# Optimization experiments

Hardware: AMD Instinct MI355X
Metric: run time of the kernel (lower is better)

Reference implementation:

```python
import jax, jax.numpy as jnp
import numpy as np

D_MODEL = 2048
N_HEADS = 16
N_KV_HEADS = 4
D_K = D_MODEL // N_HEADS          # 128
N_REP = N_HEADS // N_KV_HEADS     # 4
MAX_SEQ_LEN = 2048


def _rope_tables():
    # Matches torch Rotary: d_k//4 geometric freqs followed by d_k//4 zeros.
    freqs = (1.0 / 10000.0) ** jnp.linspace(0.0, 1.0, D_K // 4, dtype=jnp.float32)
    freqs = jnp.concatenate([freqs, jnp.zeros(D_K // 4, dtype=jnp.float32)])
    t = jnp.arange(MAX_SEQ_LEN, dtype=jnp.float32)
    theta = t[:, None] * freqs[None, :]          # [max_seq_len, d_k//2]
    return jnp.cos(theta), jnp.sin(theta)


def _apply_rotary(x, cos, sin):
    # Faithful to original: x is (B, H, T, D) and the table is indexed by
    # x.size(-3) == H (the original code rotates per-HEAD, broadcast over time).
    H = x.shape[1]
    c = cos[None, :H, None, :]
    s = sin[None, :H, None, :]
    xf = x.astype(jnp.float32)
    x1, x2 = jnp.split(xf, 2, axis=-1)
    y1 = x1 * c + x2 * s
    y2 = -x1 * s + x2 * c
    return jnp.concatenate([y1, y2], axis=-1).astype(x.dtype)


def setup_inputs() -> dict:
    key = jax.random.key(0)
    ks = jax.random.split(key, 5)
    B, T = 2, 2048
    scale = 1.0 / np.sqrt(D_MODEL)
    x = jax.random.normal(ks[0], (B, T, D_MODEL), dtype=jnp.float32)
    wq = jax.random.normal(ks[1], (N_HEADS * D_K, D_MODEL), dtype=jnp.float32) * scale
    wk = jax.random.normal(ks[2], (N_KV_HEADS * D_K, D_MODEL), dtype=jnp.float32) * scale
    wv = jax.random.normal(ks[3], (N_KV_HEADS * D_K, D_MODEL), dtype=jnp.float32) * scale
    wo = jax.random.normal(ks[4], (D_MODEL, D_MODEL), dtype=jnp.float32) * scale
    return {"x": x, "wq": wq, "wk": wk, "wv": wv, "wo": wo}


def reference(x, wq, wk, wv, wo):
    B, T, _ = x.shape
    cos, sin = _rope_tables()

    Q = (x @ wq.T).reshape(B, T, N_HEADS, D_K).transpose(0, 2, 1, 3)      # (B,Hq,T,D)
    K = (x @ wk.T).reshape(B, T, N_KV_HEADS, D_K).transpose(0, 2, 1, 3)   # (B,Hkv,T,D)
    V = (x @ wv.T).reshape(B, T, N_KV_HEADS, D_K).transpose(0, 2, 1, 3)

    Q = _apply_rotary(Q, cos, sin)
    K = _apply_rotary(K, cos, sin)

    # repeat_interleave over head dim to match query heads
    K = jnp.repeat(K, N_REP, axis=1)   # (B,Hq,T,D)
    V = jnp.repeat(V, N_REP, axis=1)

    scale = 1.0 / jnp.sqrt(jnp.asarray(D_K, dtype=jnp.float32))
    scores = jnp.einsum('bhqd,bhkd->bhqk', Q, K) * scale
    causal = jnp.tril(jnp.ones((T, T), dtype=bool))
    scores = jnp.where(causal[None, None, :, :], scores, jnp.finfo(scores.dtype).min)
    attn = jax.nn.softmax(scores, axis=-1)
    out = jnp.einsum('bhqk,bhkd->bhqd', attn, V)          # (B,Hq,T,D)
    out = out.transpose(0, 2, 1, 3).reshape(B, T, D_MODEL)
    return out @ wo.T
```

## Files before the change

### kernel.cpp

```cpp
#include <hip/hip_runtime.h>
#include <cstdint>
#include <cstddef>

typedef __attribute__((ext_vector_type(8))) short bf16x8;
typedef __attribute__((ext_vector_type(4))) float f32x4;
typedef __attribute__((ext_vector_type(16))) float f32x16;
typedef unsigned short ushort_t;

#define MFMA_BF16(a, b, c) __builtin_amdgcn_mfma_f32_16x16x32_bf16((a), (b), (c), 0, 0, 0)
#define MFMA32_BF16(a, b, c) __builtin_amdgcn_mfma_f32_32x32x16_bf16((a), (b), (c), 0, 0, 0)

__device__ __forceinline__ unsigned short f2bf(float f) {
  unsigned int u = __float_as_uint(f);
  u += 0x7fffu + ((u >> 16) & 1u);
  return (unsigned short)(u >> 16);
}
__device__ __forceinline__ float bf2f(unsigned short h) {
  return __uint_as_float(((unsigned int)h) << 16);
}
__device__ __forceinline__ float exp2_fast(float x) {
  float r;
  asm("v_exp_f32 %0, %1" : "=v"(r) : "v"(x));
  return r;
}
__device__ __forceinline__ uint32_t cvtpk_bf16(float lo, float hi) {
  uint32_t r;
  asm("v_cvt_pk_bf16_f32 %0, %1, %2" : "=v"(r) : "v"(lo), "v"(hi));
  return r;
}

__device__ __forceinline__ void gload_lds16(const void* g, void* lds) {
  __builtin_amdgcn_global_load_lds(
      (const __attribute__((address_space(1))) void*)g,
      (__attribute__((address_space(3))) void*)lds, 16, 0, 0);
}

__global__ __launch_bounds__(256)
void cvt_kernel(const float* __restrict__ x, const float* __restrict__ wq,
                const float* __restrict__ wk, const float* __restrict__ wv,
                const float* __restrict__ wo,
                ushort_t* __restrict__ xb, ushort_t* __restrict__ wqb,
                ushort_t* __restrict__ wkb, ushort_t* __restrict__ wvb,
                ushort_t* __restrict__ wob) {
  const float* src; ushort_t* dst; int n;
  switch (blockIdx.y) {
    case 0:  src = x;  dst = xb;  n = 8388608; break;
    case 1:  src = wq; dst = wqb; n = 4194304; break;
    case 2:  src = wk; dst = wkb; n = 1048576; break;
    case 3:  src = wv; dst = wvb; n = 1048576; break;
    default: src = wo; dst = wob; n = 4194304; break;
  }
  const int i = (int)(blockIdx.x * 256u + threadIdx.x) * 4;
  if (i >= n) return;
  const float4 v = *(const float4*)(src + i);
  union { unsigned short us[4]; unsigned long long u64; } pk;
  pk.us[0] = f2bf(v.x); pk.us[1] = f2bf(v.y);
  pk.us[2] = f2bf(v.z); pk.us[3] = f2bf(v.w);
  *(unsigned long long*)(dst + i) = pk.u64;
}

__global__ __launch_bounds__(256, 2)
void gemm_qkv(const ushort_t* __restrict__ A,
              const ushort_t* __restrict__ WQ, const ushort_t* __restrict__ WK,
              const ushort_t* __restrict__ WV,
              ushort_t* __restrict__ Qb, ushort_t* __restrict__ Kb,
              ushort_t* __restrict__ Vtb) {
  __shared__ bf16x8 smem_v[4096];
  char* smem = (char*)smem_v;
  const int tid  = threadIdx.x;
  const int lane = tid & 63;
  const int wave = tid >> 6;
  const int wr = wave >> 1, wc = wave & 1;
  const int y = blockIdx.y;
  int mode, ylocal;
  const ushort_t* Bsel;
  if (y < 16)      { mode = 0; ylocal = y;      Bsel = WQ; }
  else if (y < 20) { mode = 1; ylocal = y - 16; Bsel = WK; }
  else             { mode = 2; ylocal = y - 20; Bsel = WV; }
  const ushort_t* Abase = A + (size_t)blockIdx.x * 128 * 2048;
  const ushort_t* Bbase = Bsel + (size_t)ylocal * 128 * 2048;

  f32x4 acc[4][4] = {};

  #pragma unroll
  for (int it = 0; it < 4; ++it) {
    const int chunk = it * 4 + wave;
    const int r  = chunk * 8 + (lane >> 3);
    const int cg = (lane & 7) ^ (r & 7);
    gload_lds16(Abase + (size_t)r * 2048 + cg * 8, smem + chunk * 1024);
    gload_lds16(Bbase + (size_t)r * 2048 + cg * 8, smem + 16384 + chunk * 1024);
  }
  __syncthreads();

  for (int t = 0; t < 32; ++t) {
    if (t + 1 < 32) {
      char* dst = smem + ((t + 1) & 1) * 32768;
      const int k0 = (t + 1) * 64;
      #pragma unroll
      for (int it = 0; it < 4; ++it) {
        const int chunk = it * 4 + wave;
        const int r  = chunk * 8 + (lane >> 3);
        const int cg = (lane & 7) ^ (r & 7);
        gload_lds16(Abase + (size_t)r * 2048 + k0 + cg * 8, dst + chunk * 1024);
        gload_lds16(Bbase + (size_t)r * 2048 + k0 + cg * 8, dst + 16384 + chunk * 1024);
      }
    }

    char* As = smem + (t & 1) * 32768;
    char* Bs = As + 16384;
    bf16x8 af[2][4], bf_[2][4];
    #pragma unroll
    for (int kki = 0; kki < 2; ++kki) {
      #pragma unroll
      for (int m = 0; m < 4; ++m) {
        const int row = wr * 64 + m * 16 + (lane & 15);
        const int cg  = ((kki << 2) + (lane >> 4)) ^ (row & 7);
        af[kki][m] = *(const bf16x8*)(As + row * 128 + cg * 16);
      }
      #pragma unroll
      for (int n = 0; n < 4; ++n) {
        const int row = wc * 64 + n * 16 + (lane & 15);
        const int cg  = ((kki << 2) + (lane >> 4)) ^ (row & 7);
        bf_[kki][n] = *(const bf16x8*)(Bs + row * 128 + cg * 16);
      }
    }
    #pragma unroll
    for (int kki = 0; kki < 2; ++kki)
      #pragma unroll
      for (int m = 0; m < 4; ++m)
        #pragma unroll
        for (int n = 0; n < 4; ++n)
          acc[m][n] = MFMA_BF16(af[kki][m], bf_[kki][n], acc[m][n]);

    __syncthreads();
  }

  const int row0 = blockIdx.x * 128 + wr * 64;
  const int col0 = ylocal * 128 + wc * 64;
  #pragma unroll
  for (int m = 0; m < 4; ++m) {
    #pragma unroll
    for (int n = 0; n < 4; ++n) {
      #pragma unroll
      for (int j = 0; j < 4; ++j) {
        const int gm = row0 + m * 16 + ((lane >> 4) << 2) + j;
        const int gn = col0 + n * 16 + (lane & 15);
        const float v = acc[m][n][j];
        if (mode == 0) {
          Qb[(size_t)gm * 2048 + gn] = f2bf(v);
        } else if (mode == 1) {
          Kb[(size_t)gm * 512 + gn] = f2bf(v);
        } else {
          const int bb = gm >> 11, t2 = gm & 2047;
          Vtb[(size_t)bb * 512 * 2048 + (size_t)gn * 2048 + t2] = f2bf(v);
        }
      }
    }
  }
}

template<int WMODE>
__global__ __launch_bounds__(256, 2)
void gemm_bt(const ushort_t* __restrict__ A, const ushort_t* __restrict__ B,
             void* __restrict__ Cout, int M, int N, int K) {
  __shared__ bf16x8 smem_v[4096];
  char* smem = (char*)smem_v;
  const int tid  = threadIdx.x;
  const int lane = tid & 63;
  const int wave = tid >> 6;
  const int wr = wave >> 1, wc = wave & 1;
  const ushort_t* Abase = A + (size_t)blockIdx.x * 128 * K;
  const ushort_t* Bbase = B + (size_t)blockIdx.y * 128 * K;

  f32x4 acc[4][4] = {};
  const int nk = K >> 6;

  #pragma unroll
  for (int it = 0; it < 4; ++it) {
    const int chunk = it * 4 + wave;
    const int r  = chunk * 8 + (lane >> 3);
    const int cg = (lane & 7) ^ (r & 7);
    gload_lds16(Abase + (size_t)r * K + cg * 8, smem + chunk * 1024);
    gload_lds16(Bbase + (size_t)r * K + cg * 8, smem + 16384 + chunk * 1024);
  }
  __syncthreads();

  for (int t = 0; t < nk; ++t) {
    if (t + 1 < nk) {
      char* dst = smem + ((t + 1) & 1) * 32768;
      const int k0 = (t + 1) * 64;
      #pragma unroll
      for (int it = 0; it < 4; ++it) {
        const int chunk = it * 4 + wave;
        const int r  = chunk * 8 + (lane >> 3);
        const int cg = (lane & 7) ^ (r & 7);
        gload_lds16(Abase + (size_t)r * K + k0 + cg * 8, dst + chunk * 1024);
        gload_lds16(Bbase + (size_t)r * K + k0 + cg * 8, dst + 16384 + chunk * 1024);
      }
    }

    char* As = smem + (t & 1) * 32768;
    char* Bs = As + 16384;
    bf16x8 af[2][4], bf_[2][4];
    #pragma unroll
    for (int kki = 0; kki < 2; ++kki) {
      #pragma unroll
      for (int m = 0; m < 4; ++m) {
        const int row = wr * 64 + m * 16 + (lane & 15);
        const int cg  = ((kki << 2) + (lane >> 4)) ^ (row & 7);
        af[kki][m] = *(const bf16x8*)(As + row * 128 + cg * 16);
      }
      #pragma unroll
      for (int n = 0; n < 4; ++n) {
        const int row = wc * 64 + n * 16 + (lane & 15);
        const int cg  = ((kki << 2) + (lane >> 4)) ^ (row & 7);
        bf_[kki][n] = *(const bf16x8*)(Bs + row * 128 + cg * 16);
      }
    }
    #pragma unroll
    for (int kki = 0; kki < 2; ++kki)
      #pragma unroll
      for (int m = 0; m < 4; ++m)
        #pragma unroll
        for (int n = 0; n < 4; ++n)
          acc[m][n] = MFMA_BF16(af[kki][m], bf_[kki][n], acc[m][n]);

    __syncthreads();
  }

  const int row0 = blockIdx.x * 128 + wr * 64;
  const int col0 = blockIdx.y * 128 + wc * 64;
  #pragma unroll
  for (int m = 0; m < 4; ++m) {
    #pragma unroll
    for (int n = 0; n < 4; ++n) {
      #pragma unroll
      for (int j = 0; j < 4; ++j) {
        const int gm = row0 + m * 16 + ((lane >> 4) << 2) + j;
        const int gn = col0 + n * 16 + (lane & 15);
        const float v = acc[m][n][j];
        if (WMODE == 0) {
          ((ushort_t*)Cout)[(size_t)gm * N + gn] = f2bf(v);
        } else if (WMODE == 1) {
          ((float*)Cout)[(size_t)gm * N + gn] = v;
        } else {
          const int bb = gm >> 11, t2 = gm & 2047;
          ((ushort_t*)Cout)[(size_t)bb * N * 2048 + (size_t)gn * 2048 + t2] = f2bf(v);
        }
      }
    }
  }
}

__global__ __launch_bounds__(256)
void rope_k_kernel(ushort_t* __restrict__ K) {
  const int idx = blockIdx.x * 256 + threadIdx.x;
  const int NK = 4096 * 4 * 32;
  if (idx >= NK) return;
  const int t = idx >> 7, r = idx & 127;
  const int h = r >> 5, i = r & 31;
  ushort_t* p = K + (size_t)t * 512 + h * 128;
  const float f  = powf(10000.0f, -(float)i / 31.0f);
  const float th = (float)h * f;
  float sn, cs;
  sincosf(th, &sn, &cs);
  const float x1 = bf2f(p[i]), x2 = bf2f(p[i + 64]);
  p[i]      = f2bf(x1 * cs + x2 * sn);
  p[i + 64] = f2bf(-x1 * sn + x2 * cs);
}

__global__ __launch_bounds__(256, 2)
void attn_kernel(const ushort_t* __restrict__ Q, const ushort_t* __restrict__ K,
                 const ushort_t* __restrict__ Vt, ushort_t* __restrict__ AO) {
  __shared__ bf16x8 smem_v[4096];
  char* smem = (char*)smem_v;
  const int tid  = threadIdx.x;
  const int lane = tid & 63;
  const int wq   = tid >> 6;
  const int ql   = lane & 31;
  const int hi   = lane >> 5;

  const int lin = (int)blockIdx.x + 16 * (int)blockIdx.y + 256 * (int)blockIdx.z;
  const int xcd = lin & 7;
  const int s   = lin >> 3;
  const int b   = xcd >> 2;
  const int kh  = xcd & 3;
  const int h   = (kh << 2) + (s & 3);
  const int s4  = s >> 2;
  const int qt  = (s4 < 8) ? s4 : (23 - s4);

  const int q0b = qt * 128;
  const int qmin_w = q0b + wq * 32;
  const int qmax_w = qmin_w + 31;
  const int qrow = qmin_w + ql;

  const ushort_t* Qp = Q  + (size_t)b * 2048 * 2048 + (size_t)h  * 128;
  const ushort_t* Kp = K  + (size_t)b * 2048 * 512  + (size_t)kh * 128;
  const ushort_t* Vp = Vt + (size_t)b * 512 * 2048  + (size_t)kh * 128 * 2048;

  const int ntiles = (qt + 1) * 2;

  int offK[4], offV[4], ldK[4], ldV[4];
  #pragma unroll
  for (int it = 0; it < 4; ++it) {
    const int ck = it * 4 + wq;
    const int rK = ck * 4 + (lane >> 4);
    const int gK = (lane & 15) ^ (rK & 7);
    offK[it] = rK * 512 + gK * 8;  ldK[it] = ck * 1024;
    const int rV = ck * 8 + (lane >> 3);
    const int gV = (lane & 7) ^ (rV & 7);
    offV[it] = rV * 2048 + gV * 8; ldV[it] = 16384 + ck * 1024;
  }

  #pragma unroll
  for (int it = 0; it < 4; ++it) {
    gload_lds16(Kp + offK[it], smem + ldK[it]);
    gload_lds16(Vp + offV[it], smem + ldV[it]);
  }

  const float SCL = 0.08838834764831845f * 1.4426950408889634f;
  bf16x8 qf[8];
  #pragma unroll
  for (int ks = 0; ks < 8; ++ks)
    qf[ks] = *(const bf16x8*)(Qp + (size_t)qrow * 2048 + ks * 16 + hi * 8);
  #pragma unroll
  for (int ks = 0; ks < 2; ++ks) {
    union { bf16x8 v; ushort_t us[8]; } X1, X2;
    X1.v = qf[ks]; X2.v = qf[ks + 4];
    #pragma unroll
    for (int e = 0; e < 8; ++e) {
      const int i = ks * 16 + hi * 8 + e;
      const float f = __expf(-(float)i * (9.2103403720f / 31.0f));
      float sn, cs;
      sincosf((float)h * f, &sn, &cs);
      const float x1 = bf2f(X1.us[e]), x2 = bf2f(X2.us[e]);
      X1.us[e] = f2bf((x1 * cs + x2 * sn) * SCL);
      X2.us[e] = f2bf((-x1 * sn + x2 * cs) * SCL);
    }
    qf[ks] = X1.v; qf[ks + 4] = X2.v;
  }
  #pragma unroll
  for (int ks = 2; ks < 4; ++ks) {
    union { bf16x8 v; ushort_t us[8]; } X1, X2;
    X1.v = qf[ks]; X2.v = qf[ks + 4];
    #pragma unroll
    for (int e = 0; e < 8; ++e) {
      X1.us[e] = f2bf(bf2f(X1.us[e]) * SCL);
      X2.us[e] = f2bf(bf2f(X2.us[e]) * SCL);
    }
    qf[ks] = X1.v; qf[ks + 4] = X2.v;
  }

  float m_ = -3.0e38f, l_ = 0.f;
  f32x16 oacc[4] = {};

  __syncthreads();

  for (int ti = 0; ti < ntiles; ++ti) {
    const int kv0 = ti * 64;
    if (ti + 1 < ntiles) {
      const ushort_t* Kt = Kp + (size_t)(kv0 + 64) * 512;
      const ushort_t* Vn = Vp + (kv0 + 64);
      char* dst = smem + ((ti + 1) & 1) * 32768;
      #pragma unroll
      for (int it = 0; it < 4; ++it) {
        gload_lds16(Kt + offK[it], dst + ldK[it]);
        gload_lds16(Vn + offV[it], dst + ldV[it]);
      }
    }

    char* Ks = smem + (ti & 1) * 32768;
    char* Vs = Ks + 16384;
    if (kv0 <= qmax_w) {
      f32x16 sacc[2] = {};
      __builtin_amdgcn_s_setprio(1);
      #pragma unroll
      for (int kg = 0; kg < 2; ++kg) {
        const int key = kg * 32 + ql;
        #pragma unroll
        for (int ks = 0; ks < 8; ++ks) {
          const int g = ((ks << 1) + hi) ^ (key & 7);
          const bf16x8 kf = *(const bf16x8*)(Ks + key * 256 + g * 16);
          sacc[kg] = MFMA32_BF16(kf, qf[ks], sacc[kg]);
        }
      }
      __builtin_amdgcn_s_setprio(0);

      bf16x8 vfr[4][4];
      #pragma unroll
      for (int dg = 0; dg < 4; ++dg) {
        const int d = dg * 32 + ql;
        #pragma unroll
        for (int ks = 0; ks < 4; ++ks) {
          const int g = ((ks << 1) + hi) ^ (d & 7);
          vfr[dg][ks] = *(const bf16x8*)(Vs + d * 128 + g * 16);
        }
      }

      if (kv0 + 63 > qmin_w) {
        #pragma unroll
        for (int kg = 0; kg < 2; ++kg)
          #pragma unroll
          for (int r = 0; r < 16; ++r) {
            const int keyg = kv0 + kg * 32 + (r & 3) + 8 * (r >> 2) + 4 * hi;
            if (keyg > qrow) sacc[kg][r] = -3.0e38f;
          }
      }

      float mx[8];
      #pragma unroll
      for (int i = 0; i < 8; ++i) {
        const int kg = i >> 2, base = (i & 3) * 4;
        mx[i] = fmaxf(fmaxf(sacc[kg][base], sacc[kg][base + 1]),
                      fmaxf(sacc[kg][base + 2], sacc[kg][base + 3]));
      }
      float pm = fmaxf(fmaxf(fmaxf(mx[0], mx[1]), fmaxf(mx[2], mx[3])),
                       fmaxf(fmaxf(mx[4], mx[5]), fmaxf(mx[6], mx[7])));
      pm = fmaxf(pm, __shfl_xor(pm, 32));

      if (__any(pm > m_ + 11.0f)) {
        const float mn = fmaxf(m_, pm);
        const float alpha = exp2_fast(m_ - mn);
        m_ = mn;
        l_ *= alpha;
        #pragma unroll
        for (int r = 0; r < 16; ++r) {
          const float ar = __shfl(alpha, (r & 3) + 8 * (r >> 2) + 4 * hi);
          #pragma unroll
          for (int dg = 0; dg < 4; ++dg) oacc[dg][r] *= ar;
        }
      }

      float rs0 = 0.f, rs1 = 0.f, rs2 = 0.f, rs3 = 0.f;
      #pragma unroll
      for (int kg = 0; kg < 2; ++kg)
        #pragma unroll
        for (int r = 0; r < 16; r += 4) {
          const float p0 = exp2_fast(sacc[kg][r]     - m_);
          const float p1 = exp2_fast(sacc[kg][r + 1] - m_);
          const float p2 = exp2_fast(sacc[kg][r + 2] - m_);
          const float p3 = exp2_fast(sacc[kg][r + 3] - m_);
          sacc[kg][r] = p0; sacc[kg][r + 1] = p1;
          sacc[kg][r + 2] = p2; sacc[kg][r + 3] = p3;
          rs0 += p0; rs1 += p1; rs2 += p2; rs3 += p3;
        }
      float rs = (rs0 + rs1) + (rs2 + rs3);
      rs += __shfl_xor(rs, 32);
      l_ += rs;

      bf16x8 pa[4];
      #pragma unroll
      for (int ks = 0; ks < 4; ++ks) {
        const int kg = ks >> 1;
        const int base = 8 * (ks & 1);
        union { uint32_t w[4]; bf16x8 v; } U;
        #pragma unroll
        for (int j = 0; j < 2; ++j) {
          uint32_t a  = cvtpk_bf16(sacc[kg][base + 2 * j],     sacc[kg][base + 2 * j + 1]);
          uint32_t bb = cvtpk_bf16(sacc[kg][base + 4 + 2 * j], sacc[kg][base + 4 + 2 * j + 1]);
          asm volatile("v_permlane32_swap_b32 %0, %1" : "+v"(a), "+v"(bb));
          U.w[j] = a; U.w[2 + j] = bb;
        }
        pa[ks] = U.v;
      }

      __builtin_amdgcn_s_setprio(1);
      #pragma unroll
      for (int dg = 0; dg < 4; ++dg)
        #pragma unroll
        for (int ks = 0; ks < 4; ++ks)
          oacc[dg] = MFMA32_BF16(pa[ks], vfr[dg][ks], oacc[dg]);
      __builtin_amdgcn_s_setprio(0);
    }

    __syncthreads();
  }

  const float linv = 1.0f / l_;
  ushort_t* AOp = AO + (size_t)b * 2048 * 2048 + (size_t)h * 128;
  #pragma unroll
  for (int r = 0; r < 16; ++r) {
    const int cr = (r & 3) + 8 * (r >> 2) + 4 * hi;
    const float li = __shfl(linv, cr);
    const int row = q0b + wq * 32 + cr;
    #pragma unroll
    for (int dg = 0; dg < 4; ++dg)
      AOp[(size_t)row * 2048 + dg * 32 + ql] = f2bf(oacc[dg][r] * li);
  }
}

extern "C" void kernel_launch(void* const* d_in, const int* in_sizes, int n_in,
                              void* d_out, int out_size, void* d_ws, size_t ws_size,
                              hipStream_t stream) {
  const float* x  = (const float*)d_in[0];
  const float* wq = (const float*)d_in[1];
  const float* wk = (const float*)d_in[2];
  const float* wv = (const float*)d_in[3];
  const float* wo = (const float*)d_in[4];
  float* out = (float*)d_out;
  char* ws = (char*)d_ws;

  ushort_t* xb  = (ushort_t*)(ws);
  ushort_t* wqb = (ushort_t*)(ws + 16777216);
  ushort_t* wkb = (ushort_t*)(ws + 25165824);
  ushort_t* wvb = (ushort_t*)(ws + 27262976);
  ushort_t* wob = (ushort_t*)(ws + 29360128);
  ushort_t* Qb  = (ushort_t*)(ws + 37748736);
  ushort_t* Kb  = (ushort_t*)(ws + 54525952);
  ushort_t* Vtb = (ushort_t*)(ws + 58720256);
  ushort_t* AOb = (ushort_t*)(ws + 62914560);

  cvt_kernel<<<dim3(8192, 5), 256, 0, stream>>>(x, wq, wk, wv, wo,
                                                xb, wqb, wkb, wvb, wob);
  gemm_qkv<<<dim3(32, 24), 256, 0, stream>>>(xb, wqb, wkb, wvb, Qb, Kb, Vtb);
  rope_k_kernel<<<dim3(2048), 256, 0, stream>>>(Kb);
  attn_kernel<<<dim3(16, 16, 2), 256, 0, stream>>>(Qb, Kb, Vtb, AOb);
  gemm_bt<1><<<dim3(32, 16), 256, 0, stream>>>(AOb, wob, out, 4096, 2048, 2048);
}
```

Baseline: 187.6 us.

## Pair light and heavy causal query tiles in one 512-thread attention block

Each attention block now runs 8 waves: four handle query tile j and four handle its mirror tile 15-j, so every block does the same causal work and the two groups share one K/V tile stream through LDS. The grid shrinks from 512 blocks of 256 threads to 256 blocks of 512 threads, and each wave loads half as many K/V chunks. V fragments are now read from LDS inside the PV MFMA loop instead of being preloaded, which lowers register pressure for the single-block occupancy target. The trade-off is fewer, larger blocks, and the light-tile waves sit idle through the later KV tiles while still joining every barrier.

Measured after the change: 191.0 us. About the same (+1.8%).

```diff
diff --git a/kernel.cpp b/kernel.cpp
--- a/kernel.cpp
+++ b/kernel.cpp
@@ -269,7 +269,7 @@
   p[i + 64] = f2bf(-x1 * sn + x2 * cs);
 }
 
-__global__ __launch_bounds__(256, 2)
+__global__ __launch_bounds__(512, 1)
 void attn_kernel(const ushort_t* __restrict__ Q, const ushort_t* __restrict__ K,
                  const ushort_t* __restrict__ Vt, ushort_t* __restrict__ AO) {
   __shared__ bf16x8 smem_v[4096];
@@ -277,20 +277,22 @@
   const int tid  = threadIdx.x;
   const int lane = tid & 63;
   const int wq   = tid >> 6;
+  const int wsub = wq & 3;
   const int ql   = lane & 31;
   const int hi   = lane >> 5;
 
-  const int lin = (int)blockIdx.x + 16 * (int)blockIdx.y + 256 * (int)blockIdx.z;
+  const int lin = (int)blockIdx.x;
   const int xcd = lin & 7;
-  const int s   = lin >> 3;
   const int b   = xcd >> 2;
   const int kh  = xcd & 3;
+  const int s   = lin >> 3;
   const int h   = (kh << 2) + (s & 3);
-  const int s4  = s >> 2;
-  const int qt  = (s4 < 8) ? s4 : (23 - s4);
-
-  const int q0b = qt * 128;
-  const int qmin_w = q0b + wq * 32;
+  const int j   = s >> 2;
+  const int qt_hi = 15 - j;
+  const int wqt = (wq < 4) ? j : qt_hi;
+
+  const int q0b = wqt * 128;
+  const int qmin_w = q0b + wsub * 32;
   const int qmax_w = qmin_w + 31;
   const int qrow = qmin_w + ql;
 
@@ -298,12 +300,12 @@
   const ushort_t* Kp = K  + (size_t)b * 2048 * 512  + (size_t)kh * 128;
   const ushort_t* Vp = Vt + (size_t)b * 512 * 2048  + (size_t)kh * 128 * 2048;
 
-  const int ntiles = (qt + 1) * 2;
-
-  int offK[4], offV[4], ldK[4], ldV[4];
-  #pragma unroll
-  for (int it = 0; it < 4; ++it) {
-    const int ck = it * 4 + wq;
+  const int ntiles = (qt_hi + 1) * 2;
+
+  int offK[2], offV[2], ldK[2], ldV[2];
+  #pragma unroll
+  for (int it = 0; it < 2; ++it) {
+    const int ck = wq * 2 + it;
     const int rK = ck * 4 + (lane >> 4);
     const int gK = (lane & 15) ^ (rK & 7);
     offK[it] = rK * 512 + gK * 8;  ldK[it] = ck * 1024;
@@ -313,7 +315,7 @@
   }
 
   #pragma unroll
-  for (int it = 0; it < 4; ++it) {
+  for (int it = 0; it < 2; ++it) {
     gload_lds16(Kp + offK[it], smem + ldK[it]);
     gload_lds16(Vp + offV[it], smem + ldV[it]);
   }
@@ -363,7 +365,7 @@
       const ushort_t* Vn = Vp + (kv0 + 64);
       char* dst = smem + ((ti + 1) & 1) * 32768;
       #pragma unroll
-      for (int it = 0; it < 4; ++it) {
+      for (int it = 0; it < 2; ++it) {
         gload_lds16(Kt + offK[it], dst + ldK[it]);
         gload_lds16(Vn + offV[it], dst + ldV[it]);
       }
@@ -385,17 +387,6 @@
         }
       }
       __builtin_amdgcn_s_setprio(0);
-
-      bf16x8 vfr[4][4];
-      #pragma unroll
-      for (int dg = 0; dg < 4; ++dg) {
-        const int d = dg * 32 + ql;
-        #pragma unroll
-        for (int ks = 0; ks < 4; ++ks) {
-          const int g = ((ks << 1) + hi) ^ (d & 7);
-          vfr[dg][ks] = *(const bf16x8*)(Vs + d * 128 + g * 16);
-        }
-      }
 
       if (kv0 + 63 > qmin_w) {
         #pragma unroll
@@ -455,21 +446,26 @@
         const int base = 8 * (ks & 1);
         union { uint32_t w[4]; bf16x8 v; } U;
         #pragma unroll
-        for (int j = 0; j < 2; ++j) {
-          uint32_t a  = cvtpk_bf16(sacc[kg][base + 2 * j],     sacc[kg][base + 2 * j + 1]);
-          uint32_t bb = cvtpk_bf16(sacc[kg][base + 4 + 2 * j], sacc[kg][base + 4 + 2 * j + 1]);
+        for (int jj = 0; jj < 2; ++jj) {
+          uint32_t a  = cvtpk_bf16(sacc[kg][base + 2 * jj],     sacc[kg][base + 2 * jj + 1]);
+          uint32_t bb = cvtpk_bf16(sacc[kg][base + 4 + 2 * jj], sacc[kg][base + 4 + 2 * jj + 1]);
           asm volatile("v_permlane32_swap_b32 %0, %1" : "+v"(a), "+v"(bb));
-          U.w[j] = a; U.w[2 + j] = bb;
+          U.w[jj] = a; U.w[2 + jj] = bb;
         }
         pa[ks] = U.v;
       }
 
       __builtin_amdgcn_s_setprio(1);
       #pragma unroll
-      for (int dg = 0; dg < 4; ++dg)
-        #pragma unroll
-        for (int ks = 0; ks < 4; ++ks)
-          oacc[dg] = MFMA32_BF16(pa[ks], vfr[dg][ks], oacc[dg]);
+      for (int dg = 0; dg < 4; ++dg) {
+        const int d = dg * 32 + ql;
+        #pragma unroll
+        for (int ks = 0; ks < 4; ++ks) {
+          const int g = ((ks << 1) + hi) ^ (d & 7);
+          const bf16x8 vf = *(const bf16x8*)(Vs + d * 128 + g * 16);
+          oacc[dg] = MFMA32_BF16(pa[ks], vf, oacc[dg]);
+        }
+      }
       __builtin_amdgcn_s_setprio(0);
     }
 
@@ -482,7 +478,7 @@
   for (int r = 0; r < 16; ++r) {
     const int cr = (r & 3) + 8 * (r >> 2) + 4 * hi;
     const float li = __shfl(linv, cr);
-    const int row = q0b + wq * 32 + cr;
+    const int row = q0b + wsub * 32 + cr;
     #pragma unroll
     for (int dg = 0; dg < 4; ++dg)
       AOp[(size_t)row * 2048 + dg * 32 + ql] = f2bf(oacc[dg][r] * li);
@@ -514,6 +510,6 @@
                                                 xb, wqb, wkb, wvb, wob);
   gemm_qkv<<<dim3(32, 24), 256, 0, stream>>>(xb, wqb, wkb, wvb, Qb, Kb, Vtb);
   rope_k_kernel<<<dim3(2048), 256, 0, stream>>>(Kb);
-  attn_kernel<<<dim3(16, 16, 2), 256, 0, stream>>>(Qb, Kb, Vtb, AOb);
+  attn_kernel<<<dim3(256), 512, 0, stream>>>(Qb, Kb, Vtb, AOb);
   gemm_bt<1><<<dim3(32, 16), 256, 0, stream>>>(AOb, wob, out, 4096, 2048, 2048);
 }
```
